# Kernel optimization log

Hardware: AMD Instinct MI355X
Metric: run time of the kernel (lower is better)

The kernel has to match this reference:

```python
import jax, jax.numpy as jnp
import numpy as np

B, T, E, H, DEPTH = 128, 256, 512, 1024, 3


def setup_inputs() -> dict:
    key = jax.random.key(0)
    ks = jax.random.split(key, 9)
    s_e = 1.0 / np.sqrt(E)
    s_h = 1.0 / np.sqrt(H)
    return {
        "x": jax.random.normal(ks[0], (B, T, E), jnp.float32),
        "W_ih0": jax.random.normal(ks[1], (4 * H, E), jnp.float32) * s_e,
        "W_hh0": jax.random.normal(ks[2], (4 * H, H), jnp.float32) * s_h,
        "b_ih0": jax.random.normal(ks[3], (4 * H,), jnp.float32) * s_h,
        "b_hh0": jax.random.normal(ks[4], (4 * H,), jnp.float32) * s_h,
        "W_ih_r": jax.random.normal(ks[5], (DEPTH - 1, 4 * H, H), jnp.float32) * s_h,
        "W_hh_r": jax.random.normal(ks[6], (DEPTH - 1, 4 * H, H), jnp.float32) * s_h,
        "b_ih_r": jax.random.normal(ks[7], (DEPTH - 1, 4 * H), jnp.float32) * s_h,
        "b_hh_r": jax.random.normal(ks[8], (DEPTH - 1, 4 * H), jnp.float32) * s_h,
        "trainable": 1,
    }


def _lstm_cell(inp, h, c, Wih, Whh, bih, bhh):
    # torch.nn.LSTMCell: gates = inp @ Wih.T + bih + h @ Whh.T + bhh; order i,f,g,o
    gates = inp @ Wih.T + bih + h @ Whh.T + bhh
    i, f, g, o = jnp.split(gates, 4, axis=-1)
    c_new = jax.nn.sigmoid(f) * c + jax.nn.sigmoid(i) * jnp.tanh(g)
    h_new = jax.nn.sigmoid(o) * jnp.tanh(c_new)
    return h_new, c_new


def reference(x, W_ih0, W_hh0, b_ih0, b_hh0, W_ih_r, W_hh_r, b_ih_r, b_hh_r, trainable):
    b, _, _ = x.shape
    h_dim = W_hh0.shape[1]
    n_rest = W_ih_r.shape[0]
    zeros = jnp.zeros((b, h_dim), x.dtype)
    x_t = jnp.swapaxes(x, 0, 1)  # [T, B, E]

    def step(carry, xt):
        hs, cs = carry  # each [n_rest, B, H]
        # faithful bug: layer-0 state is never updated -> always zeros
        h, c = _lstm_cell(xt, zeros, zeros, W_ih0, W_hh0, b_ih0, b_hh0)
        new_h, new_c = [], []
        for l in range(n_rest):  # small fixed depth loop
            h, c = _lstm_cell(h, hs[l], cs[l], W_ih_r[l], W_hh_r[l], b_ih_r[l], b_hh_r[l])
            new_h.append(h)
            new_c.append(c)
        return (jnp.stack(new_h), jnp.stack(new_c)), h

    init = (jnp.zeros((n_rest, b, h_dim), x.dtype),
            jnp.zeros((n_rest, b, h_dim), x.dtype))
    _, out = jax.lax.scan(step, init, x_t)
    return out  # [T, B, H] == list of top-layer h per timestep
```

## Files before the change

kernel.cpp:

```cpp
#include <hip/hip_runtime.h>

static constexpr int Bc = 128;
static constexpr int Tc = 256;
static constexpr int Ec = 512;
static constexpr int Hc = 1024;
static constexpr int SLOT = Bc * Hc;

using bf16x8 = __attribute__((ext_vector_type(8))) short;
using f32x4  = __attribute__((ext_vector_type(4))) float;

__device__ __forceinline__ unsigned short f2bf(float f) {
  unsigned int u = __float_as_uint(f);
  u += 0x7FFFu + ((u >> 16) & 1u);
  return (unsigned short)(u >> 16);
}
__device__ __forceinline__ float sigm(float x) { return 1.0f / (1.0f + __expf(-x)); }
__device__ __forceinline__ float ftanh(float x) { return 1.0f - 2.0f / (__expf(2.0f * x) + 1.0f); }

#define MFMA16(A, Bf, C) __builtin_amdgcn_mfma_f32_16x16x32_bf16((A), (Bf), (C), 0, 0, 0)

__device__ __forceinline__ void poll_rlx(const int* p, int tgt) {
  while (__hip_atomic_load(p, __ATOMIC_RELAXED, __HIP_MEMORY_SCOPE_AGENT) < tgt)
    __builtin_amdgcn_s_sleep(1);
}
__device__ __forceinline__ void poll_fast(const int* p, int tgt) {
  while (__hip_atomic_load(p, __ATOMIC_RELAXED, __HIP_MEMORY_SCOPE_AGENT) < tgt) {}
}
__device__ __forceinline__ void sig(int* p, int v) {
  __hip_atomic_store(p, v, __ATOMIC_RELAXED, __HIP_MEMORY_SCOPE_AGENT);
}
__device__ __forceinline__ void stg_c(unsigned short* p, unsigned short v) {
  __hip_atomic_store(p, v, __ATOMIC_RELAXED, __HIP_MEMORY_SCOPE_AGENT);
}
__device__ __forceinline__ bf16x8 ldg_c(const unsigned short* p) {
  union { unsigned long long u[2]; bf16x8 v; } r;
  r.u[0] = __hip_atomic_load((const unsigned long long*)p,       __ATOMIC_RELAXED, __HIP_MEMORY_SCOPE_AGENT);
  r.u[1] = __hip_atomic_load((const unsigned long long*)(p + 4), __ATOMIC_RELAXED, __HIP_MEMORY_SCOPE_AGENT);
  return r.v;
}
__device__ __forceinline__ int lds_acq(const int* p) {
  return __hip_atomic_load(p, __ATOMIC_ACQUIRE, __HIP_MEMORY_SCOPE_WORKGROUP);
}
__device__ __forceinline__ void lds_rel(int* p, int v) {
  __hip_atomic_store(p, v, __ATOMIC_RELEASE, __HIP_MEMORY_SCOPE_WORKGROUP);
}

__global__ void k_cvt_bf16(const float* __restrict__ src, unsigned short* __restrict__ dst, int n) {
  int i = (blockIdx.x * blockDim.x + threadIdx.x) * 4;
  if (i + 3 < n) {
    f32x4 v = *(const f32x4*)(src + i);
    *(ushort4*)(dst + i) = make_ushort4(f2bf(v[0]), f2bf(v[1]), f2bf(v[2]), f2bf(v[3]));
  }
}

__global__ void k_prep_small(const float* __restrict__ bih0, const float* __restrict__ bhh0,
                             float* __restrict__ b0s,
                             unsigned short* __restrict__ h2c,
                             int* __restrict__ f1, int* __restrict__ f2) {
  int i = blockIdx.x * blockDim.x + threadIdx.x;
  if (i < 4096) b0s[i] = bih0[i] + bhh0[i];
  h2c[i] = 0;
  if (i < 128 * 16) { f1[i] = 0; f2[i] = 0; }
}

__global__ __launch_bounds__(256, 1) void k_l0(
    const unsigned short* __restrict__ xb, const unsigned short* __restrict__ W0,
    const float* __restrict__ b0s, unsigned short* __restrict__ H0)
{
  __shared__ unsigned short Axs[64 * 128 * 8];
  const int tid = threadIdx.x;
  const int lane = tid & 63, wid = tid >> 6;
  const int bx = blockIdx.x;
  const int jbase = blockIdx.y * 64 + wid * 16;
  const int ri = lane & 15, kg = lane >> 4;

  for (int i = tid; i < 8192; i += 256) {
    const int row = i >> 6;
    const int chunk = i & 63;
    const int phys = chunk * 128 + (row ^ (chunk & 15));
    *(bf16x8*)(Axs + (size_t)phys * 8) =
        *(const bf16x8*)(xb + ((size_t)row * Tc + bx) * Ec + chunk * 8);
  }
  __syncthreads();

  const int j = jbase + ri;
  const float bi = b0s[j], bg = b0s[2 * Hc + j], bo = b0s[3 * Hc + j];
  const unsigned short* w0r = W0 + ((size_t)(0 * Hc + j)) * Ec + kg * 8;
  const unsigned short* w2r = W0 + ((size_t)(2 * Hc + j)) * Ec + kg * 8;
  const unsigned short* w3r = W0 + ((size_t)(3 * Hc + j)) * Ec + kg * 8;

  f32x4 ai[8], ag[8], ao[8];
#pragma unroll
  for (int u = 0; u < 8; ++u) { ai[u] = (f32x4){0,0,0,0}; ag[u] = (f32x4){0,0,0,0}; ao[u] = (f32x4){0,0,0,0}; }

#pragma unroll 4
  for (int kk = 0; kk < Ec / 32; ++kk) {
    bf16x8 wi = *(const bf16x8*)(w0r + kk * 32);
    bf16x8 wg = *(const bf16x8*)(w2r + kk * 32);
    bf16x8 wo = *(const bf16x8*)(w3r + kk * 32);
    const int ch = kk * 4 + kg;
#pragma unroll
    for (int u = 0; u < 8; ++u) {
      const int phys = ch * 128 + ((u * 16 + ri) ^ (ch & 15));
      bf16x8 a = *(const bf16x8*)(Axs + (size_t)phys * 8);
      ai[u] = MFMA16(a, wi, ai[u]);
      ag[u] = MFMA16(a, wg, ag[u]);
      ao[u] = MFMA16(a, wo, ao[u]);
    }
  }

  unsigned short* hb = H0 + (size_t)bx * SLOT + (size_t)(j >> 3) * 1024 + (j & 7);
#pragma unroll
  for (int u = 0; u < 8; ++u) {
#pragma unroll
    for (int q = 0; q < 4; ++q) {
      const int b = u * 16 + kg * 4 + q;
      float c = sigm(ai[u][q] + bi) * ftanh(ag[u][q] + bg);
      float h = sigm(ao[u][q] + bo) * ftanh(c);
      hb[(size_t)b * 8] = f2bf(h);
    }
  }
}

__global__ __launch_bounds__(512, 1) void k_rec(
    const unsigned short* H0,
    const float* __restrict__ Wih, const float* __restrict__ Whh,
    const float* __restrict__ bih, const float* __restrict__ bhh,
    unsigned short* h1c,
    unsigned short* h2c,
    int* f1, int* f2,
    float* out)
{
  __shared__ unsigned short Wlds[2 * 64 * 64 * 8];
  __shared__ float pbuf[4][4][64][4];
  __shared__ int flg[32];
  int* sF_   = flg + 0;
  int* sG_   = flg + 4;
  int* pollF = flg + 12;
  int* doneS = flg + 16;

  const int tid = threadIdx.x;
  const int lane = tid & 63, wid = tid >> 6;
  const int m = wid & 3;
  const bool gatedw = (wid >= 4);
  const int bid = blockIdx.x;
  const int layer = bid >> 7;
  const int w = bid & 127;
  const int j0 = w * 8;
  const int ri = lane & 15, kg = lane >> 4;

  if (tid < 32) flg[tid] = 0;

  const size_t lw = (size_t)layer * 4096 * 1024;
  for (int s = tid; s < 2 * 64 * 64; s += 512) {
    const int l   = s & 63;
    const int kkg = (s >> 6) & 63;
    const int t   = s >> 12;
    const int rr  = l & 15;
    const int gate = t * 2 + (rr >> 3);
    const int R = gate * 1024 + j0 + (rr & 7);
    const int k = kkg * 32 + (l >> 4) * 8;
    const float* src = (k < 1024) ? (Wih + lw + (size_t)R * 1024 + k)
                                  : (Whh + lw + (size_t)R * 1024 + (k - 1024));
    f32x4 v0 = *(const f32x4*)src;
    f32x4 v1 = *(const f32x4*)(src + 4);
    ushort4* d = (ushort4*)(Wlds + (size_t)s * 8);
    d[0] = make_ushort4(f2bf(v0[0]), f2bf(v0[1]), f2bf(v0[2]), f2bf(v0[3]));
    d[1] = make_ushort4(f2bf(v1[0]), f2bf(v1[1]), f2bf(v1[2]), f2bf(v1[3]));
  }

  const int jme = j0 + (ri & 7);
  const int g0 = (ri < 8) ? 0 : 1;
  const int g1 = (ri < 8) ? 2 : 3;
  const float bias0 = bih[layer * 4096 + g0 * 1024 + jme] + bhh[layer * 4096 + g0 * 1024 + jme];
  const float bias1 = bih[layer * 4096 + g1 * 1024 + jme] + bhh[layer * 4096 + g1 * 1024 + jme];

  float c0[4]  = {0.f, 0.f, 0.f, 0.f};
  float c1s[4] = {0.f, 0.f, 0.f, 0.f};

  const unsigned short* lds0 = Wlds + (size_t)lane * 8;
  const unsigned short* lds1 = Wlds + (size_t)64 * 64 * 8 + (size_t)lane * 8;
  const int abase = kg * 1024 + (m * 32 + ri) * 8;
  const bool lo = (ri < 8);

  f32x4 acc00, acc01, acc10, acc11;
#define ZERO4() { acc00 = (f32x4){0,0,0,0}; acc01 = (f32x4){0,0,0,0}; \
                  acc10 = (f32x4){0,0,0,0}; acc11 = (f32x4){0,0,0,0}; }
#define PLOAD()  { acc00 = *(const f32x4*)&pbuf[m][0][lane][0]; \
                   acc01 = *(const f32x4*)&pbuf[m][1][lane][0]; \
                   acc10 = *(const f32x4*)&pbuf[m][2][lane][0]; \
                   acc11 = *(const f32x4*)&pbuf[m][3][lane][0]; }
#define PWRITE() { *(f32x4*)&pbuf[m][0][lane][0] = acc00; \
                   *(f32x4*)&pbuf[m][1][lane][0] = acc01; \
                   *(f32x4*)&pbuf[m][2][lane][0] = acc10; \
                   *(f32x4*)&pbuf[m][3][lane][0] = acc11; }

#define HALF_MM4R(Abase, LDSOFF, K0, K1)                                    \
  {                                                                         \
    const unsigned short* ap_ = (Abase) + abase;                            \
    _Pragma("unroll")                                                       \
    for (int kk = (K0); kk < (K1); ++kk) {                                  \
      bf16x8 b0 = *(const bf16x8*)(lds0 + (LDSOFF) + kk * 512);             \
      bf16x8 b1 = *(const bf16x8*)(lds1 + (LDSOFF) + kk * 512);             \
      bf16x8 vlo = *(const bf16x8*)(ap_ + kk * 4096);                       \
      bf16x8 vhi = *(const bf16x8*)(ap_ + kk * 4096 + 128);                 \
      acc00 = MFMA16(vlo, b0, acc00);                                       \
      acc01 = MFMA16(vlo, b1, acc01);                                       \
      acc10 = MFMA16(vhi, b0, acc10);                                       \
      acc11 = MFMA16(vhi, b1, acc11);                                       \
    }                                                                       \
  }

#define HALF_MM4C(Abase, LDSOFF, K0, K1)                                    \
  {                                                                         \
    const unsigned short* ap_ = (Abase) + abase;                            \
    _Pragma("unroll")                                                       \
    for (int kk = (K0); kk < (K1); ++kk) {                                  \
      bf16x8 b0 = *(const bf16x8*)(lds0 + (LDSOFF) + kk * 512);             \
      bf16x8 b1 = *(const bf16x8*)(lds1 + (LDSOFF) + kk * 512);             \
      bf16x8 vlo = ldg_c(ap_ + kk * 4096);                                  \
      bf16x8 vhi = ldg_c(ap_ + kk * 4096 + 128);                            \
      acc00 = MFMA16(vlo, b0, acc00);                                       \
      acc01 = MFMA16(vlo, b1, acc01);                                       \
      acc10 = MFMA16(vhi, b0, acc10);                                       \
      acc11 = MFMA16(vhi, b1, acc11);                                       \
    }                                                                       \
  }

#define CELL4(accA, accB, cre, hnarr)                                       \
  _Pragma("unroll")                                                         \
  for (int q = 0; q < 4; ++q) {                                             \
    float x0 = accA[q] + bias0;                                             \
    float x1 = accB[q] + bias1;                                             \
    float p0 = __shfl_xor(x0, 8);                                           \
    float p1 = __shfl_xor(x1, 8);                                           \
    float gi = lo ? x0 : p0;                                                \
    float gf = lo ? p0 : x0;                                                \
    float gg = lo ? x1 : p1;                                                \
    float go = lo ? p1 : x1;                                                \
    float cn = sigm(gf) * cre[q] + sigm(gi) * ftanh(gg);                    \
    hnarr[q] = sigm(go) * ftanh(cn);                                        \
    cre[q] = cn;                                                            \
  }

#define GPOLL_BAR(farr, tgt, stamp)                                         \
  { if (lane < 32) poll_rlx((farr) + (m * 32 + lane) * 16, (tgt));          \
    if (lane == 0) lds_rel(&(stamp)[m], (tgt));                             \
    while (lds_acq(&(stamp)[0]) < (tgt) || lds_acq(&(stamp)[1]) < (tgt) ||  \
           lds_acq(&(stamp)[2]) < (tgt) || lds_acq(&(stamp)[3]) < (tgt)) {} }

  __syncthreads();

  if (layer == 0) {
    if (!gatedw) {
      ZERO4() HALF_MM4R(H0, 0, 0, 32)
      for (int t = 0; t < Tc; ++t) {
        while (lds_acq(&sG_[m]) < t) {}
        PWRITE()
        if (lane == 0) lds_rel(&sF_[m], t + 1);
        if (t + 1 < Tc) { ZERO4() HALF_MM4R(H0 + (size_t)(t + 1) * SLOT, 0, 0, 32) }
      }
    } else {
      for (int p = 0; p < Tc; ++p) {
        while (lds_acq(&sF_[m]) < p + 1) {}
        PLOAD()
        if (lane == 0) lds_rel(&sG_[m], p + 1);
        if (p >= 1) {
          const unsigned short* gb = h1c + (size_t)(p - 1) * SLOT;
#pragma unroll
          for (int g = 0; g < 4; ++g) {
            if (lane < 32) poll_fast(f1 + (g * 32 + lane) * 16, p);
            HALF_MM4R(gb, 32 * 512, 8 * g, 8 * g + 8)
          }
        }
        float hn0[4], hn1[4];
        CELL4(acc00, acc01, c0, hn0)
        CELL4(acc10, acc11, c1s, hn1)
        if (lo) {
          unsigned short* hb = h1c + (size_t)p * SLOT + (size_t)w * 1024 + (ri & 7);
#pragma unroll
          for (int q = 0; q < 4; ++q) {
            const int r0 = m * 32 + kg * 4 + q;
            stg_c(hb + (size_t)r0 * 8, f2bf(hn0[q]));
            stg_c(hb + (size_t)(r0 + 16) * 8, f2bf(hn1[q]));
          }
        }
        __asm__ volatile("s_waitcnt vmcnt(0)" ::: "memory");
        if (lane == 0) lds_rel(&doneS[m], p + 1);
        if (m == 0) {
          while (lds_acq(&doneS[1]) < p + 1 || lds_acq(&doneS[2]) < p + 1 ||
                 lds_acq(&doneS[3]) < p + 1) {}
          if (lane == 0) sig(f1 + w * 16, p + 1);
        }
      }
    }
  } else {
    if (!gatedw) {
      GPOLL_BAR(f1, 1, pollF)
      ZERO4() HALF_MM4R(h1c, 0, 0, 32)
      for (int t = 0; t < Tc; ++t) {
        while (lds_acq(&sG_[m]) < t) {}
        PWRITE()
        if (lane == 0) lds_rel(&sF_[m], t + 1);
        if (t + 1 < Tc) {
          GPOLL_BAR(f1, t + 2, pollF)
          ZERO4() HALF_MM4R(h1c + (size_t)(t + 1) * SLOT, 0, 0, 32)
        }
      }
    } else {
      for (int s = 0; s < Tc; ++s) {
        while (lds_acq(&sF_[m]) < s + 1) {}
        PLOAD()
        if (lane == 0) lds_rel(&sG_[m], s + 1);
        {
          const unsigned short* gb = h2c + (size_t)((s - 1) & 3) * SLOT;
#pragma unroll
          for (int g = 0; g < 4; ++g) {
            if (s >= 1 && lane < 32) poll_fast(f2 + (g * 32 + lane) * 16, s);
            HALF_MM4C(gb, 32 * 512, 8 * g, 8 * g + 8)
          }
        }
        float hn0[4], hn1[4];
        CELL4(acc00, acc01, c0, hn0)
        CELL4(acc10, acc11, c1s, hn1)
        if (lo) {
          unsigned short* hb = h2c + (size_t)(s & 3) * SLOT + (size_t)w * 1024 + (ri & 7);
#pragma unroll
          for (int q = 0; q < 4; ++q) {
            const int r0 = m * 32 + kg * 4 + q;
            stg_c(hb + (size_t)r0 * 8, f2bf(hn0[q]));
            stg_c(hb + (size_t)(r0 + 16) * 8, f2bf(hn1[q]));
          }
        }
        __asm__ volatile("s_waitcnt vmcnt(0)" ::: "memory");
        if (lane == 0) lds_rel(&doneS[m], s + 1);
        if (m == 0) {
          while (lds_acq(&doneS[1]) < s + 1 || lds_acq(&doneS[2]) < s + 1 ||
                 lds_acq(&doneS[3]) < s + 1) {}
          if (lane == 0) sig(f2 + w * 16, s + 1);
        }
        if (lo) {
          float* po = out + (size_t)s * SLOT;
#pragma unroll
          for (int q = 0; q < 4; ++q) {
            const int r0 = m * 32 + kg * 4 + q;
            po[(size_t)r0 * Hc + jme] = hn0[q];
            po[(size_t)(r0 + 16) * Hc + jme] = hn1[q];
          }
        }
      }
    }
  }
}

extern "C" void kernel_launch(void* const* d_in, const int* in_sizes, int n_in,
                              void* d_out, int out_size, void* d_ws, size_t ws_size,
                              hipStream_t stream) {
  const float* x     = (const float*)d_in[0];
  const float* W_ih0 = (const float*)d_in[1];
  const float* b_ih0 = (const float*)d_in[3];
  const float* b_hh0 = (const float*)d_in[4];
  const float* W_ihr = (const float*)d_in[5];
  const float* W_hhr = (const float*)d_in[6];
  const float* b_ihr = (const float*)d_in[7];
  const float* b_hhr = (const float*)d_in[8];

  char* ws = (char*)d_ws;
  constexpr size_t H0_OFF  = 0;
  constexpr size_t H2B_OFF = H0_OFF + (size_t)Tc * SLOT * 2;
  constexpr size_t F1_OFF  = H2B_OFF + (size_t)4 * SLOT * 2;
  constexpr size_t F2_OFF  = F1_OFF + 128 * 16 * 4;

  unsigned short* H0  = (unsigned short*)(ws + H0_OFF);
  unsigned short* h2c = (unsigned short*)(ws + H2B_OFF);
  float* b0s = (float*)(ws + F2_OFF + 128 * 16 * 4);
  int* f1 = (int*)(ws + F1_OFF);
  int* f2 = (int*)(ws + F2_OFF);

  unsigned short* xb  = (unsigned short*)d_out;
  unsigned short* W0b = (unsigned short*)d_out + (size_t)Bc * Tc * Ec;
  unsigned short* h1c = (unsigned short*)d_out + (size_t)Tc * SLOT;
  float* out = (float*)d_out;

  int n0 = 4096 * 512;
  k_cvt_bf16<<<n0 / 1024, 256, 0, stream>>>(W_ih0, W0b, n0);
  int nx = Bc * Tc * Ec;
  k_cvt_bf16<<<nx / 1024, 256, 0, stream>>>(x, xb, nx);
  k_prep_small<<<2048, 256, 0, stream>>>(b_ih0, b_hh0, b0s, h2c, f1, f2);
  k_l0<<<dim3(Tc, 16), 256, 0, stream>>>(xb, W0b, b0s, H0);

  k_rec<<<dim3(256), dim3(512), 0, stream>>>(H0, W_ihr, W_hhr, b_ihr, b_hhr,
                                             h1c, h2c, f1, f2, out);
}
```

Baseline: 3.818 ms.

## Use per-wave progress flags instead of intra-block barrier before global signal

Each wave now publishes its own global progress flag (512 flags per layer instead of 128), which removes the LDS doneS barrier where wave 0 waited for its siblings before signalling. Consumers poll two flags per lane and stagger the group order by block index to spread polling traffic. The gate-waiting waves now poll and compute per group instead of waiting on a full block poll barrier. This shortens the cross-block dependency chain in the persistent recurrent kernel, at the cost of four times as many flag reads.

```diff
diff --git a/kernel.cpp b/kernel.cpp
--- a/kernel.cpp
+++ b/kernel.cpp
@@ -60,7 +60,7 @@
   int i = blockIdx.x * blockDim.x + threadIdx.x;
   if (i < 4096) b0s[i] = bih0[i] + bhh0[i];
   h2c[i] = 0;
-  if (i < 128 * 16) { f1[i] = 0; f2[i] = 0; }
+  if (i < 512 * 16) { f1[i] = 0; f2[i] = 0; }
 }
 
 __global__ __launch_bounds__(256, 1) void k_l0(
@@ -133,11 +133,9 @@
 {
   __shared__ unsigned short Wlds[2 * 64 * 64 * 8];
   __shared__ float pbuf[4][4][64][4];
-  __shared__ int flg[32];
-  int* sF_   = flg + 0;
-  int* sG_   = flg + 4;
-  int* pollF = flg + 12;
-  int* doneS = flg + 16;
+  __shared__ int flg[16];
+  int* sF_ = flg + 0;
+  int* sG_ = flg + 4;
 
   const int tid = threadIdx.x;
   const int lane = tid & 63, wid = tid >> 6;
@@ -149,7 +147,7 @@
   const int j0 = w * 8;
   const int ri = lane & 15, kg = lane >> 4;
 
-  if (tid < 32) flg[tid] = 0;
+  if (tid < 16) flg[tid] = 0;
 
   const size_t lw = (size_t)layer * 4096 * 1024;
   for (int s = tid; s < 2 * 64 * 64; s += 512) {
@@ -182,6 +180,8 @@
   const unsigned short* lds1 = Wlds + (size_t)64 * 64 * 8 + (size_t)lane * 8;
   const int abase = kg * 1024 + (m * 32 + ri) * 8;
   const bool lo = (ri < 8);
+  const int pw = lane & 31;
+  const int wv = (lane >> 5) * 2;
 
   f32x4 acc00, acc01, acc10, acc11;
 #define ZERO4() { acc00 = (f32x4){0,0,0,0}; acc01 = (f32x4){0,0,0,0}; \
@@ -243,11 +243,14 @@
     cre[q] = cn;                                                            \
   }
 
-#define GPOLL_BAR(farr, tgt, stamp)                                         \
-  { if (lane < 32) poll_rlx((farr) + (m * 32 + lane) * 16, (tgt));          \
-    if (lane == 0) lds_rel(&(stamp)[m], (tgt));                             \
-    while (lds_acq(&(stamp)[0]) < (tgt) || lds_acq(&(stamp)[1]) < (tgt) ||  \
-           lds_acq(&(stamp)[2]) < (tgt) || lds_acq(&(stamp)[3]) < (tgt)) {} }
+#define GPOLL_FAST(farr, grp, tgt)                                          \
+  { const int* base_ = (farr) + (((grp) * 32 + pw) * 4 + wv) * 16;          \
+    poll_fast(base_, (tgt));                                                \
+    poll_fast(base_ + 16, (tgt)); }
+#define GPOLL_SLEEP(farr, grp, tgt)                                         \
+  { const int* base_ = (farr) + (((grp) * 32 + pw) * 4 + wv) * 16;          \
+    poll_rlx(base_, (tgt));                                                 \
+    poll_rlx(base_ + 16, (tgt)); }
 
   __syncthreads();
 
@@ -268,8 +271,9 @@
         if (p >= 1) {
           const unsigned short* gb = h1c + (size_t)(p - 1) * SLOT;
 #pragma unroll
-          for (int g = 0; g < 4; ++g) {
-            if (lane < 32) poll_fast(f1 + (g * 32 + lane) * 16, p);
+          for (int gi = 0; gi < 4; ++gi) {
+            const int g = (gi + w) & 3;
+            GPOLL_FAST(f1, g, p)
             HALF_MM4R(gb, 32 * 512, 8 * g, 8 * g + 8)
           }
         }
@@ -286,25 +290,29 @@
           }
         }
         __asm__ volatile("s_waitcnt vmcnt(0)" ::: "memory");
-        if (lane == 0) lds_rel(&doneS[m], p + 1);
-        if (m == 0) {
-          while (lds_acq(&doneS[1]) < p + 1 || lds_acq(&doneS[2]) < p + 1 ||
-                 lds_acq(&doneS[3]) < p + 1) {}
-          if (lane == 0) sig(f1 + w * 16, p + 1);
-        }
+        if (lane == 0) sig(f1 + (w * 4 + m) * 16, p + 1);
       }
     }
   } else {
     if (!gatedw) {
-      GPOLL_BAR(f1, 1, pollF)
-      ZERO4() HALF_MM4R(h1c, 0, 0, 32)
+      ZERO4()
+#pragma unroll
+      for (int g = 0; g < 4; ++g) {
+        GPOLL_SLEEP(f1, g, 1)
+        HALF_MM4R(h1c, 0, 8 * g, 8 * g + 8)
+      }
       for (int t = 0; t < Tc; ++t) {
         while (lds_acq(&sG_[m]) < t) {}
         PWRITE()
         if (lane == 0) lds_rel(&sF_[m], t + 1);
         if (t + 1 < Tc) {
-          GPOLL_BAR(f1, t + 2, pollF)
-          ZERO4() HALF_MM4R(h1c + (size_t)(t + 1) * SLOT, 0, 0, 32)
+          ZERO4()
+          const unsigned short* nb = h1c + (size_t)(t + 1) * SLOT;
+#pragma unroll
+          for (int g = 0; g < 4; ++g) {
+            GPOLL_SLEEP(f1, g, t + 2)
+            HALF_MM4R(nb, 0, 8 * g, 8 * g + 8)
+          }
         }
       }
     } else {
@@ -315,8 +323,9 @@
         {
           const unsigned short* gb = h2c + (size_t)((s - 1) & 3) * SLOT;
 #pragma unroll
-          for (int g = 0; g < 4; ++g) {
-            if (s >= 1 && lane < 32) poll_fast(f2 + (g * 32 + lane) * 16, s);
+          for (int gi = 0; gi < 4; ++gi) {
+            const int g = (gi + w) & 3;
+            if (s >= 1) GPOLL_FAST(f2, g, s)
             HALF_MM4C(gb, 32 * 512, 8 * g, 8 * g + 8)
           }
         }
@@ -333,12 +342,7 @@
           }
         }
         __asm__ volatile("s_waitcnt vmcnt(0)" ::: "memory");
-        if (lane == 0) lds_rel(&doneS[m], s + 1);
-        if (m == 0) {
-          while (lds_acq(&doneS[1]) < s + 1 || lds_acq(&doneS[2]) < s + 1 ||
-                 lds_acq(&doneS[3]) < s + 1) {}
-          if (lane == 0) sig(f2 + w * 16, s + 1);
-        }
+        if (lane == 0) sig(f2 + (w * 4 + m) * 16, s + 1);
         if (lo) {
           float* po = out + (size_t)s * SLOT;
 #pragma unroll
@@ -369,11 +373,11 @@
   constexpr size_t H0_OFF  = 0;
   constexpr size_t H2B_OFF = H0_OFF + (size_t)Tc * SLOT * 2;
   constexpr size_t F1_OFF  = H2B_OFF + (size_t)4 * SLOT * 2;
-  constexpr size_t F2_OFF  = F1_OFF + 128 * 16 * 4;
+  constexpr size_t F2_OFF  = F1_OFF + 512 * 16 * 4;
 
   unsigned short* H0  = (unsigned short*)(ws + H0_OFF);
   unsigned short* h2c = (unsigned short*)(ws + H2B_OFF);
-  float* b0s = (float*)(ws + F2_OFF + 128 * 16 * 4);
+  float* b0s = (float*)(ws + F2_OFF + 512 * 16 * 4);
   int* f1 = (int*)(ws + F1_OFF);
   int* f2 = (int*)(ws + F2_OFF);
 
```

Result: slower. 4.531 ms (+18.7%).
